# Kernel optimization log

Hardware: AMD Instinct MI355X
Metric: run time of the kernel (lower is better)

The kernel has to match this reference:

```python
import jax, jax.numpy as jnp
import numpy as np

RANGE_EXTENDER = 5.0
EPS = 1e-8  # torch cosine_similarity eps

N_CLASSES = 256
LATENT = 256
H = W = 256


def setup_inputs() -> dict:
    key = jax.random.key(0)
    k1, k2, k3 = jax.random.split(key, 3)
    x = jax.random.normal(k1, (LATENT, H, W), dtype=jnp.float32)
    weights = jax.random.normal(k2, (N_CLASSES, LATENT), dtype=jnp.float32)
    scale = jax.random.normal(k3, (N_CLASSES,), dtype=jnp.float32)
    return {"x": x, "weights": weights, "scale": scale}


def reference(x, weights, scale):
    # out[c,i,j] = cos_sim(x[:,i,j], weights[c]) * scale[c] * RANGE_EXTENDER
    x_norm = jnp.sqrt(jnp.sum(x * x, axis=0, keepdims=True))           # (1, H, W)
    xn = x / jnp.maximum(x_norm, EPS)                                   # (D, H, W)
    w_norm = jnp.sqrt(jnp.sum(weights * weights, axis=1, keepdims=True))  # (C, 1)
    wn = weights / jnp.maximum(w_norm, EPS)                             # (C, D)
    cos = jnp.einsum("cd,dhw->chw", wn, xn)                            # (C, H, W)
    return cos * scale[:, None, None] * RANGE_EXTENDER
```

## Files before the change

kernel.cpp:

```cpp
#include <hip/hip_runtime.h>
#include <stdint.h>

typedef unsigned short u16;
typedef __bf16 bf16_t;
typedef bf16_t bf16x8 __attribute__((ext_vector_type(8)));
typedef float f32x4 __attribute__((ext_vector_type(4)));

static constexpr int P = 65536;

__device__ __forceinline__ float bfbits2f(uint32_t b) {
    union { uint32_t i; float f; } u; u.i = b << 16; return u.f;
}
__device__ __forceinline__ u16 f2bf(float f) {
    union { float f; uint32_t i; } u; u.f = f;
    uint32_t x = u.i + 0x7FFFu + ((u.i >> 16) & 1u);
    return (u16)(x >> 16);
}
__device__ __forceinline__ uint32_t pack2(float a, float b) {
    return (uint32_t)f2bf(a) | ((uint32_t)f2bf(b) << 16);
}

__device__ __forceinline__ int detect_bf16_input(const void* Xg) {
    const uint32_t* Xu = (const uint32_t*)Xg;
    const int lane = (int)(threadIdx.x & 63);
    const uint32_t v = Xu[(size_t)lane * 131071u];
    const uint32_t e = (v >> 7) & 0xFFu;
    unsigned long long m = __ballot(e >= 96u && e <= 135u);
    return __popcll(m) >= 40;
}

__global__ __launch_bounds__(64) void coshead_prep(
    const void* __restrict__ Xg, const void* __restrict__ Wg,
    const void* __restrict__ Sg, float* __restrict__ rs_ws,
    u16* __restrict__ wbf)
{
    const int c    = (int)blockIdx.x;
    const int lane = (int)threadIdx.x;
    const int bf   = detect_bf16_input(Xg);
    float s;
    uint2 packed;
    if (bf) {
        const uint2 v = *(const uint2*)((const u16*)Wg + (size_t)c * 256 + lane * 4);
        const float a = bfbits2f(v.x & 0xFFFFu), b = bfbits2f(v.x >> 16);
        const float d = bfbits2f(v.y & 0xFFFFu), e = bfbits2f(v.y >> 16);
        s = a * a + b * b + d * d + e * e;
        packed = v;
    } else {
        const f32x4 v = *(const f32x4*)((const float*)Wg + (size_t)c * 256 + lane * 4);
        s = v[0] * v[0] + v[1] * v[1] + v[2] * v[2] + v[3] * v[3];
        packed.x = pack2(v[0], v[1]);
        packed.y = pack2(v[2], v[3]);
    }
    *(uint2*)(wbf + (size_t)c * 256 + lane * 4) = packed;
    s += __shfl_xor(s, 1);  s += __shfl_xor(s, 2);  s += __shfl_xor(s, 4);
    s += __shfl_xor(s, 8);  s += __shfl_xor(s, 16); s += __shfl_xor(s, 32);
    if (lane == 0) {
        const float sc = bf ? bfbits2f((uint32_t)((const u16*)Sg)[c])
                            : ((const float*)Sg)[c];
        rs_ws[c] = sc * 5.0f / fmaxf(sqrtf(s), 1e-8f);
    }
}

__global__ __launch_bounds__(256, 3) void coshead_gemm(
    const void* __restrict__ Xg_, const u16* __restrict__ Wbf,
    const float* __restrict__ rs_ws, float* __restrict__ Og)
{
    __shared__ char smem_[32768 + 8192];
    char* sA = smem_;
    char* sB = smem_ + 32768;

    const int t  = (int)threadIdx.x;
    const int l  = t & 63;
    const int w  = t >> 6;
    const int p0 = (int)blockIdx.x * 64;
    const int bf = detect_bf16_input(Xg_);

    const int g    = t & 7;
    const int r    = t >> 3;
    const int m16  = l & 15;
    const int quad = l >> 4;

    const int lrow = l >> 3;
    const int gsl  = (l & 7) ^ lrow;
    const u16* wsrc = Wbf + ((size_t)(w * 8 + lrow) << 8) + gsl * 8;
    char* ldsA = sA + w * 1024;

    float ssq[8];
#pragma unroll
    for (int j = 0; j < 8; ++j) ssq[j] = 0.f;
    f32x4 acc[4][4];
#pragma unroll
    for (int a = 0; a < 4; ++a)
#pragma unroll
        for (int b = 0; b < 4; ++b)
#pragma unroll
            for (int i = 0; i < 4; ++i) acc[a][b][i] = 0.f;

    for (int kc = 0; kc < 4; ++kc) {
#pragma unroll
        for (int j = 0; j < 8; ++j) {
            __builtin_amdgcn_global_load_lds(
                (const __attribute__((address_space(1))) void*)(wsrc + j * 8192 + kc * 64),
                (__attribute__((address_space(3))) void*)(ldsA + j * 4096),
                16, 0, 0);
        }

        if (bf) {
            const u16* xp = (const u16*)Xg_ + (size_t)(2 * r + kc * 64) * P + p0 + g * 8;
            const uint4 v0 = *(const uint4*)xp;
            const uint4 v1 = *(const uint4*)(xp + P);
            const uint32_t e0[4] = {v0.x, v0.y, v0.z, v0.w};
            const uint32_t e1[4] = {v1.x, v1.y, v1.z, v1.w};
#pragma unroll
            for (int d = 0; d < 4; ++d) {
                const float f00 = bfbits2f(e0[d] & 0xFFFFu), f01 = bfbits2f(e0[d] >> 16);
                const float f10 = bfbits2f(e1[d] & 0xFFFFu), f11 = bfbits2f(e1[d] >> 16);
                ssq[2 * d]     += f00 * f00 + f10 * f10;
                ssq[2 * d + 1] += f01 * f01 + f11 * f11;
                const uint32_t d0 = (e0[d] & 0xFFFFu) | (e1[d] << 16);
                const uint32_t d1 = (e0[d] >> 16) | (e1[d] & 0xFFFF0000u);
                const int pj0 = g * 8 + 2 * d, pj1 = pj0 + 1;
                *(uint32_t*)(sB + pj0 * 128 + (((r >> 2) ^ (pj0 & 7) ^ g) * 16) + (r & 3) * 4) = d0;
                *(uint32_t*)(sB + pj1 * 128 + (((r >> 2) ^ (pj1 & 7) ^ g) * 16) + (r & 3) * 4) = d1;
            }
        } else {
            const float* xp = (const float*)Xg_ + (size_t)(2 * r + kc * 64) * P + p0 + g * 8;
            const f32x4 c0  = *(const f32x4*)xp;
            const f32x4 c1  = *(const f32x4*)(xp + 4);
            const f32x4 d0v = *(const f32x4*)(xp + P);
            const f32x4 d1v = *(const f32x4*)(xp + P + 4);
            const float f0[8] = {c0[0], c0[1], c0[2], c0[3], c1[0], c1[1], c1[2], c1[3]};
            const float f1[8] = {d0v[0], d0v[1], d0v[2], d0v[3], d1v[0], d1v[1], d1v[2], d1v[3]};
#pragma unroll
            for (int j = 0; j < 8; ++j) {
                ssq[j] += f0[j] * f0[j] + f1[j] * f1[j];
                const int pix = g * 8 + j;
                *(uint32_t*)(sB + pix * 128 + (((r >> 2) ^ (pix & 7) ^ g) * 16) + (r & 3) * 4) =
                    pack2(f0[j], f1[j]);
            }
        }
        __syncthreads();

#pragma unroll
        for (int kk = 0; kk < 2; ++kk) {
            bf16x8 af[4], bfr[4];
#pragma unroll
            for (int tm = 0; tm < 4; ++tm) {
                const int row = w * 64 + tm * 16 + m16;
                af[tm] = *(const bf16x8*)(sA + row * 128 + (((kk * 4 + quad) ^ (row & 7)) * 16));
            }
#pragma unroll
            for (int tn = 0; tn < 4; ++tn) {
                const int pix = tn * 16 + m16;
                bfr[tn] = *(const bf16x8*)(sB + pix * 128 +
                           (((kk * 4 + quad) ^ (pix & 7) ^ (pix >> 3)) * 16));
            }
#pragma unroll
            for (int tm = 0; tm < 4; ++tm)
#pragma unroll
                for (int tn = 0; tn < 4; ++tn)
                    acc[tm][tn] = __builtin_amdgcn_mfma_f32_16x16x32_bf16(
                        af[tm], bfr[tn], acc[tm][tn], 0, 0, 0);
        }
        __syncthreads();
    }

    float* xs   = (float*)sA;
    float* xinv = (float*)sB;
#pragma unroll
    for (int j = 0; j < 8; ++j) xs[r * 64 + g * 8 + j] = ssq[j];
    __syncthreads();
    if (t < 64) {
        float sx = 0.f;
#pragma unroll
        for (int rr = 0; rr < 32; ++rr) sx += xs[rr * 64 + t];
        xinv[t] = 1.0f / fmaxf(sqrtf(sx), 1e-8f);
    }
    __syncthreads();

    float inv4[4];
#pragma unroll
    for (int tn = 0; tn < 4; ++tn) inv4[tn] = xinv[tn * 16 + m16];
#pragma unroll
    for (int tm = 0; tm < 4; ++tm) {
        const int cbase = w * 64 + tm * 16 + quad * 4;
        const f32x4 rs4 = *(const f32x4*)(rs_ws + cbase);
#pragma unroll
        for (int tn = 0; tn < 4; ++tn) {
#pragma unroll
            for (int i = 0; i < 4; ++i) {
                Og[(size_t)(cbase + i) * P + p0 + tn * 16 + m16] =
                    acc[tm][tn][i] * rs4[i] * inv4[tn];
            }
        }
    }
}

extern "C" void kernel_launch(void* const* d_in, const int* in_sizes, int n_in,
                              void* d_out, int out_size, void* d_ws, size_t ws_size,
                              hipStream_t stream) {
    (void)out_size; (void)ws_size;
    const void* X = d_in[0];
    const void* W = d_in[1];
    const void* S = d_in[2];
    for (int i = 0; i < n_in; ++i) {
        if (in_sizes[i] == 256 * 65536) X = d_in[i];
        else if (in_sizes[i] == 256 * 256) W = d_in[i];
        else if (in_sizes[i] == 256)      S = d_in[i];
    }
    float* rs  = (float*)d_ws;
    u16*   wbf = (u16*)((char*)d_ws + 1024);
    coshead_prep<<<dim3(256), dim3(64), 0, stream>>>(X, W, S, rs, wbf);
    coshead_gemm<<<dim3(1024), dim3(256), 0, stream>>>(X, wbf, rs, (float*)d_out);
}
```

Before: 134.8 us.

## Double-buffer fp32 X tiles via async LDS loads and read W fragments from global

```diff
diff --git a/kernel.cpp b/kernel.cpp
--- a/kernel.cpp
+++ b/kernel.cpp
@@ -65,9 +65,7 @@
     const void* __restrict__ Xg_, const u16* __restrict__ Wbf,
     const float* __restrict__ rs_ws, float* __restrict__ Og)
 {
-    __shared__ char smem_[32768 + 8192];
-    char* sA = smem_;
-    char* sB = smem_ + 32768;
+    __shared__ char smem_[49152];
 
     const int t  = (int)threadIdx.x;
     const int l  = t & 63;
@@ -80,11 +78,6 @@
     const int m16  = l & 15;
     const int quad = l >> 4;
 
-    const int lrow = l >> 3;
-    const int gsl  = (l & 7) ^ lrow;
-    const u16* wsrc = Wbf + ((size_t)(w * 8 + lrow) << 8) + gsl * 8;
-    char* ldsA = sA + w * 1024;
-
     float ssq[8];
 #pragma unroll
     for (int j = 0; j < 8; ++j) ssq[j] = 0.f;
@@ -96,16 +89,109 @@
 #pragma unroll
             for (int i = 0; i < 4; ++i) acc[a][b][i] = 0.f;
 
-    for (int kc = 0; kc < 4; ++kc) {
-#pragma unroll
-        for (int j = 0; j < 8; ++j) {
-            __builtin_amdgcn_global_load_lds(
-                (const __attribute__((address_space(1))) void*)(wsrc + j * 8192 + kc * 64),
-                (__attribute__((address_space(3))) void*)(ldsA + j * 4096),
-                16, 0, 0);
-        }
-
-        if (bf) {
+    if (!bf) {
+        char* ring = smem_;
+        char* sBd  = smem_ + 32768;
+
+        const int lrow16 = l >> 4;
+        const int lpix4  = (l & 15) * 4;
+        const float* xsrc0 = (const float*)Xg_ + (size_t)(w * 16 + lrow16) * P + p0 + lpix4;
+
+        const u16* wrow = Wbf + (size_t)(w * 64 + m16) * 256 + quad * 8;
+
+        {
+            const float* s0 = xsrc0;
+            char* db = ring + w * 4096;
+#pragma unroll
+            for (int j = 0; j < 4; ++j) {
+                __builtin_amdgcn_global_load_lds(
+                    (const __attribute__((address_space(1))) void*)(s0 + (size_t)(j * 4) * P),
+                    (__attribute__((address_space(3))) void*)(db + j * 1024),
+                    16, 0, 0);
+            }
+        }
+
+        for (int kc = 0; kc < 4; ++kc) {
+            const int cur = kc & 1;
+            asm volatile("s_waitcnt vmcnt(0)" ::: "memory");
+            __builtin_amdgcn_sched_barrier(0);
+            __builtin_amdgcn_s_barrier();
+
+            bf16x8 afr[2][4];
+#pragma unroll
+            for (int kk = 0; kk < 2; ++kk)
+#pragma unroll
+                for (int tm = 0; tm < 4; ++tm)
+                    afr[kk][tm] = *(const bf16x8*)(wrow + kc * 64 + kk * 32 + tm * 4096);
+            if (kc < 3) {
+                const float* s1 = xsrc0 + (size_t)((kc + 1) * 64) * P;
+                char* db = ring + (cur ^ 1) * 16384 + w * 4096;
+#pragma unroll
+                for (int j = 0; j < 4; ++j) {
+                    __builtin_amdgcn_global_load_lds(
+                        (const __attribute__((address_space(1))) void*)(s1 + (size_t)(j * 4) * P),
+                        (__attribute__((address_space(3))) void*)(db + j * 1024),
+                        16, 0, 0);
+                }
+            }
+
+            {
+                const char* rg = ring + cur * 16384;
+                const int ro = (2 * r) * 256 + g * 32;
+                const f32x4 c0  = *(const f32x4*)(rg + ro);
+                const f32x4 c1  = *(const f32x4*)(rg + ro + 16);
+                const f32x4 d0v = *(const f32x4*)(rg + ro + 256);
+                const f32x4 d1v = *(const f32x4*)(rg + ro + 256 + 16);
+                const float f0[8] = {c0[0], c0[1], c0[2], c0[3], c1[0], c1[1], c1[2], c1[3]};
+                const float f1[8] = {d0v[0], d0v[1], d0v[2], d0v[3], d1v[0], d1v[1], d1v[2], d1v[3]};
+                char* sBw = sBd + cur * 8192;
+#pragma unroll
+                for (int j = 0; j < 8; ++j) {
+                    ssq[j] += f0[j] * f0[j] + f1[j] * f1[j];
+                    const int pix = g * 8 + j;
+                    *(uint32_t*)(sBw + pix * 128 + (((r >> 2) ^ (pix & 7) ^ g) * 16) + (r & 3) * 4) =
+                        pack2(f0[j], f1[j]);
+                }
+            }
+            asm volatile("s_waitcnt lgkmcnt(0)" ::: "memory");
+            __builtin_amdgcn_sched_barrier(0);
+            __builtin_amdgcn_s_barrier();
+
+            const char* sBw = sBd + cur * 8192;
+#pragma unroll
+            for (int kk = 0; kk < 2; ++kk) {
+                bf16x8 bfr[4];
+#pragma unroll
+                for (int tn = 0; tn < 4; ++tn) {
+                    const int pix = tn * 16 + m16;
+                    bfr[tn] = *(const bf16x8*)(sBw + pix * 128 +
+                               (((kk * 4 + quad) ^ (pix & 7) ^ (pix >> 3)) * 16));
+                }
+#pragma unroll
+                for (int tm = 0; tm < 4; ++tm)
+#pragma unroll
+                    for (int tn = 0; tn < 4; ++tn)
+                        acc[tm][tn] = __builtin_amdgcn_mfma_f32_16x16x32_bf16(
+                            afr[kk][tm], bfr[tn], acc[tm][tn], 0, 0, 0);
+            }
+        }
+        __syncthreads();
+    } else {
+        char* sA = smem_;
+        char* sB = smem_ + 32768;
+        const int lrow = l >> 3;
+        const int gsl  = (l & 7) ^ lrow;
+        const u16* wsrc = Wbf + ((size_t)(w * 8 + lrow) << 8) + gsl * 8;
+        char* ldsA = sA + w * 1024;
+
+        for (int kc = 0; kc < 4; ++kc) {
+#pragma unroll
+            for (int j = 0; j < 8; ++j) {
+                __builtin_amdgcn_global_load_lds(
+                    (const __attribute__((address_space(1))) void*)(wsrc + j * 8192 + kc * 64),
+                    (__attribute__((address_space(3))) void*)(ldsA + j * 4096),
+                    16, 0, 0);
+            }
             const u16* xp = (const u16*)Xg_ + (size_t)(2 * r + kc * 64) * P + p0 + g * 8;
             const uint4 v0 = *(const uint4*)xp;
             const uint4 v1 = *(const uint4*)(xp + P);
@@ -123,50 +209,34 @@
                 *(uint32_t*)(sB + pj0 * 128 + (((r >> 2) ^ (pj0 & 7) ^ g) * 16) + (r & 3) * 4) = d0;
                 *(uint32_t*)(sB + pj1 * 128 + (((r >> 2) ^ (pj1 & 7) ^ g) * 16) + (r & 3) * 4) = d1;
             }
-        } else {
-            const float* xp = (const float*)Xg_ + (size_t)(2 * r + kc * 64) * P + p0 + g * 8;
-            const f32x4 c0  = *(const f32x4*)xp;
-            const f32x4 c1  = *(const f32x4*)(xp + 4);
-            const f32x4 d0v = *(const f32x4*)(xp + P);
-            const f32x4 d1v = *(const f32x4*)(xp + P + 4);
-            const float f0[8] = {c0[0], c0[1], c0[2], c0[3], c1[0], c1[1], c1[2], c1[3]};
-            const float f1[8] = {d0v[0], d0v[1], d0v[2], d0v[3], d1v[0], d1v[1], d1v[2], d1v[3]};
-#pragma unroll
-            for (int j = 0; j < 8; ++j) {
-                ssq[j] += f0[j] * f0[j] + f1[j] * f1[j];
-                const int pix = g * 8 + j;
-                *(uint32_t*)(sB + pix * 128 + (((r >> 2) ^ (pix & 7) ^ g) * 16) + (r & 3) * 4) =
-                    pack2(f0[j], f1[j]);
-            }
-        }
-        __syncthreads();
-
-#pragma unroll
-        for (int kk = 0; kk < 2; ++kk) {
-            bf16x8 af[4], bfr[4];
-#pragma unroll
-            for (int tm = 0; tm < 4; ++tm) {
-                const int row = w * 64 + tm * 16 + m16;
-                af[tm] = *(const bf16x8*)(sA + row * 128 + (((kk * 4 + quad) ^ (row & 7)) * 16));
-            }
-#pragma unroll
-            for (int tn = 0; tn < 4; ++tn) {
-                const int pix = tn * 16 + m16;
-                bfr[tn] = *(const bf16x8*)(sB + pix * 128 +
-                           (((kk * 4 + quad) ^ (pix & 7) ^ (pix >> 3)) * 16));
-            }
-#pragma unroll
-            for (int tm = 0; tm < 4; ++tm)
-#pragma unroll
-                for (int tn = 0; tn < 4; ++tn)
-                    acc[tm][tn] = __builtin_amdgcn_mfma_f32_16x16x32_bf16(
-                        af[tm], bfr[tn], acc[tm][tn], 0, 0, 0);
-        }
-        __syncthreads();
-    }
-
-    float* xs   = (float*)sA;
-    float* xinv = (float*)sB;
+            __syncthreads();
+#pragma unroll
+            for (int kk = 0; kk < 2; ++kk) {
+                bf16x8 af[4], bfr[4];
+#pragma unroll
+                for (int tm = 0; tm < 4; ++tm) {
+                    const int row = w * 64 + tm * 16 + m16;
+                    af[tm] = *(const bf16x8*)(sA + row * 128 + (((kk * 4 + quad) ^ (row & 7)) * 16));
+                }
+#pragma unroll
+                for (int tn = 0; tn < 4; ++tn) {
+                    const int pix = tn * 16 + m16;
+                    bfr[tn] = *(const bf16x8*)(sB + pix * 128 +
+                               (((kk * 4 + quad) ^ (pix & 7) ^ (pix >> 3)) * 16));
+                }
+#pragma unroll
+                for (int tm = 0; tm < 4; ++tm)
+#pragma unroll
+                    for (int tn = 0; tn < 4; ++tn)
+                        acc[tm][tn] = __builtin_amdgcn_mfma_f32_16x16x32_bf16(
+                            af[tm], bfr[tn], acc[tm][tn], 0, 0, 0);
+            }
+            __syncthreads();
+        }
+    }
+
+    float* xs   = (float*)smem_;
+    float* xinv = (float*)(smem_ + 32768);
 #pragma unroll
     for (int j = 0; j < 8; ++j) xs[r * 64 + g * 8 + j] = ssq[j];
     __syncthreads();
```

Result: slower. 157.2 us (+16.6%).

## Double-buffer X tiles and read weights directly from global in fp32 path

Applied to the files above, without the earlier changes.

```diff
diff --git a/kernel.cpp b/kernel.cpp
--- a/kernel.cpp
+++ b/kernel.cpp
@@ -65,9 +65,7 @@
     const void* __restrict__ Xg_, const u16* __restrict__ Wbf,
     const float* __restrict__ rs_ws, float* __restrict__ Og)
 {
-    __shared__ char smem_[32768 + 8192];
-    char* sA = smem_;
-    char* sB = smem_ + 32768;
+    __shared__ char smem_[40960];
 
     const int t  = (int)threadIdx.x;
     const int l  = t & 63;
@@ -80,11 +78,6 @@
     const int m16  = l & 15;
     const int quad = l >> 4;
 
-    const int lrow = l >> 3;
-    const int gsl  = (l & 7) ^ lrow;
-    const u16* wsrc = Wbf + ((size_t)(w * 8 + lrow) << 8) + gsl * 8;
-    char* ldsA = sA + w * 1024;
-
     float ssq[8];
 #pragma unroll
     for (int j = 0; j < 8; ++j) ssq[j] = 0.f;
@@ -96,16 +89,92 @@
 #pragma unroll
             for (int i = 0; i < 4; ++i) acc[a][b][i] = 0.f;
 
-    for (int kc = 0; kc < 4; ++kc) {
-#pragma unroll
-        for (int j = 0; j < 8; ++j) {
-            __builtin_amdgcn_global_load_lds(
-                (const __attribute__((address_space(1))) void*)(wsrc + j * 8192 + kc * 64),
-                (__attribute__((address_space(3))) void*)(ldsA + j * 4096),
-                16, 0, 0);
-        }
-
-        if (bf) {
+    if (!bf) {
+        char* sBd = smem_;
+        const u16* wrow = Wbf + (size_t)(w * 64 + m16) * 256 + quad * 8;
+        const float* xbase = (const float*)Xg_ + (size_t)(2 * r) * P + p0 + g * 8;
+
+        {
+            const float* xp = xbase;
+            const f32x4 c0  = *(const f32x4*)xp;
+            const f32x4 c1  = *(const f32x4*)(xp + 4);
+            const f32x4 d0v = *(const f32x4*)(xp + P);
+            const f32x4 d1v = *(const f32x4*)(xp + P + 4);
+            const float f0[8] = {c0[0], c0[1], c0[2], c0[3], c1[0], c1[1], c1[2], c1[3]};
+            const float f1[8] = {d0v[0], d0v[1], d0v[2], d0v[3], d1v[0], d1v[1], d1v[2], d1v[3]};
+#pragma unroll
+            for (int j = 0; j < 8; ++j) {
+                ssq[j] += f0[j] * f0[j] + f1[j] * f1[j];
+                const int pix = g * 8 + j;
+                *(uint32_t*)(sBd + pix * 128 + (((r >> 2) ^ (pix & 7) ^ g) * 16) + (r & 3) * 4) =
+                    pack2(f0[j], f1[j]);
+            }
+        }
+
+        for (int kc = 0; kc < 4; ++kc) {
+            const int cur = kc & 1;
+            __syncthreads();
+
+            f32x4 rA, rB, rC, rD;
+            if (kc < 3) {
+                const float* xp = xbase + (size_t)((kc + 1) * 64) * P;
+                rA = *(const f32x4*)xp;
+                rB = *(const f32x4*)(xp + 4);
+                rC = *(const f32x4*)(xp + P);
+                rD = *(const f32x4*)(xp + P + 4);
+            }
+
+            const char* sBw = sBd + cur * 8192;
+#pragma unroll 1
+            for (int kk = 0; kk < 2; ++kk) {
+                bf16x8 af[4], bfr[4];
+#pragma unroll
+                for (int tm = 0; tm < 4; ++tm)
+                    af[tm] = *(const bf16x8*)(wrow + kc * 64 + kk * 32 + tm * 4096);
+#pragma unroll
+                for (int tn = 0; tn < 4; ++tn) {
+                    const int pix = tn * 16 + m16;
+                    bfr[tn] = *(const bf16x8*)(sBw + pix * 128 +
+                               (((kk * 4 + quad) ^ (pix & 7) ^ (pix >> 3)) * 16));
+                }
+#pragma unroll
+                for (int tm = 0; tm < 4; ++tm)
+#pragma unroll
+                    for (int tn = 0; tn < 4; ++tn)
+                        acc[tm][tn] = __builtin_amdgcn_mfma_f32_16x16x32_bf16(
+                            af[tm], bfr[tn], acc[tm][tn], 0, 0, 0);
+            }
+
+            if (kc < 3) {
+                const float f0[8] = {rA[0], rA[1], rA[2], rA[3], rB[0], rB[1], rB[2], rB[3]};
+                const float f1[8] = {rC[0], rC[1], rC[2], rC[3], rD[0], rD[1], rD[2], rD[3]};
+                char* sBn = sBd + (cur ^ 1) * 8192;
+#pragma unroll
+                for (int j = 0; j < 8; ++j) {
+                    ssq[j] += f0[j] * f0[j] + f1[j] * f1[j];
+                    const int pix = g * 8 + j;
+                    *(uint32_t*)(sBn + pix * 128 + (((r >> 2) ^ (pix & 7) ^ g) * 16) + (r & 3) * 4) =
+                        pack2(f0[j], f1[j]);
+                }
+            }
+        }
+        __syncthreads();
+    } else {
+        char* sA = smem_;
+        char* sB = smem_ + 32768;
+        const int lrow = l >> 3;
+        const int gsl  = (l & 7) ^ lrow;
+        const u16* wsrc = Wbf + ((size_t)(w * 8 + lrow) << 8) + gsl * 8;
+        char* ldsA = sA + w * 1024;
+
+        for (int kc = 0; kc < 4; ++kc) {
+#pragma unroll
+            for (int j = 0; j < 8; ++j) {
+                __builtin_amdgcn_global_load_lds(
+                    (const __attribute__((address_space(1))) void*)(wsrc + j * 8192 + kc * 64),
+                    (__attribute__((address_space(3))) void*)(ldsA + j * 4096),
+                    16, 0, 0);
+            }
             const u16* xp = (const u16*)Xg_ + (size_t)(2 * r + kc * 64) * P + p0 + g * 8;
             const uint4 v0 = *(const uint4*)xp;
             const uint4 v1 = *(const uint4*)(xp + P);
@@ -123,50 +192,34 @@
                 *(uint32_t*)(sB + pj0 * 128 + (((r >> 2) ^ (pj0 & 7) ^ g) * 16) + (r & 3) * 4) = d0;
                 *(uint32_t*)(sB + pj1 * 128 + (((r >> 2) ^ (pj1 & 7) ^ g) * 16) + (r & 3) * 4) = d1;
             }
-        } else {
-            const float* xp = (const float*)Xg_ + (size_t)(2 * r + kc * 64) * P + p0 + g * 8;
-            const f32x4 c0  = *(const f32x4*)xp;
-            const f32x4 c1  = *(const f32x4*)(xp + 4);
-            const f32x4 d0v = *(const f32x4*)(xp + P);
-            const f32x4 d1v = *(const f32x4*)(xp + P + 4);
-            const float f0[8] = {c0[0], c0[1], c0[2], c0[3], c1[0], c1[1], c1[2], c1[3]};
-            const float f1[8] = {d0v[0], d0v[1], d0v[2], d0v[3], d1v[0], d1v[1], d1v[2], d1v[3]};
-#pragma unroll
-            for (int j = 0; j < 8; ++j) {
-                ssq[j] += f0[j] * f0[j] + f1[j] * f1[j];
-                const int pix = g * 8 + j;
-                *(uint32_t*)(sB + pix * 128 + (((r >> 2) ^ (pix & 7) ^ g) * 16) + (r & 3) * 4) =
-                    pack2(f0[j], f1[j]);
-            }
-        }
-        __syncthreads();
-
-#pragma unroll
-        for (int kk = 0; kk < 2; ++kk) {
-            bf16x8 af[4], bfr[4];
-#pragma unroll
-            for (int tm = 0; tm < 4; ++tm) {
-                const int row = w * 64 + tm * 16 + m16;
-                af[tm] = *(const bf16x8*)(sA + row * 128 + (((kk * 4 + quad) ^ (row & 7)) * 16));
-            }
-#pragma unroll
-            for (int tn = 0; tn < 4; ++tn) {
-                const int pix = tn * 16 + m16;
-                bfr[tn] = *(const bf16x8*)(sB + pix * 128 +
-                           (((kk * 4 + quad) ^ (pix & 7) ^ (pix >> 3)) * 16));
-            }
-#pragma unroll
-            for (int tm = 0; tm < 4; ++tm)
-#pragma unroll
-                for (int tn = 0; tn < 4; ++tn)
-                    acc[tm][tn] = __builtin_amdgcn_mfma_f32_16x16x32_bf16(
-                        af[tm], bfr[tn], acc[tm][tn], 0, 0, 0);
-        }
-        __syncthreads();
-    }
-
-    float* xs   = (float*)sA;
-    float* xinv = (float*)sB;
+            __syncthreads();
+#pragma unroll
+            for (int kk = 0; kk < 2; ++kk) {
+                bf16x8 af[4], bfr[4];
+#pragma unroll
+                for (int tm = 0; tm < 4; ++tm) {
+                    const int row = w * 64 + tm * 16 + m16;
+                    af[tm] = *(const bf16x8*)(sA + row * 128 + (((kk * 4 + quad) ^ (row & 7)) * 16));
+                }
+#pragma unroll
+                for (int tn = 0; tn < 4; ++tn) {
+                    const int pix = tn * 16 + m16;
+                    bfr[tn] = *(const bf16x8*)(sB + pix * 128 +
+                               (((kk * 4 + quad) ^ (pix & 7) ^ (pix >> 3)) * 16));
+                }
+#pragma unroll
+                for (int tm = 0; tm < 4; ++tm)
+#pragma unroll
+                    for (int tn = 0; tn < 4; ++tn)
+                        acc[tm][tn] = __builtin_amdgcn_mfma_f32_16x16x32_bf16(
+                            af[tm], bfr[tn], acc[tm][tn], 0, 0, 0);
+            }
+            __syncthreads();
+        }
+    }
+
+    float* xs   = (float*)smem_;
+    float* xinv = (float*)(smem_ + 24576);
 #pragma unroll
     for (int j = 0; j < 8; ++j) xs[r * 64 + g * 8 + j] = ssq[j];
     __syncthreads();
```

New measurement: 142.7 us. +5.9%, slower.
